# Kernel tuning notes

Hardware: AMD Instinct MI355X
Metric: run time of the kernel (lower is better)

Reference implementation:

```python
import jax, jax.numpy as jnp
import numpy as np

VARIANCES = jnp.array([0.1, 0.1, 0.2, 0.2], jnp.float32)
MAX_TOTAL = 200       # max_total_size
MAX_PER_CLASS = 50    # per-class NMS cap (combined-NMS max_output_size_per_class)
IOU_THR = 0.5
SCORE_THR = 0.5       # score_threshold
EPS = 1e-8


def setup_inputs() -> dict:
    key = jax.random.key(0)
    k1, k2, kc, kh = jax.random.split(key, 4)
    B, N, C = 16, 24564, 81
    pred_deltas = jax.random.normal(k1, (B, N, 4), jnp.float32)
    pred_labels = jax.random.uniform(k2, (B, N, C), jnp.float32)
    # realistic normalized priors: centers uniform in [0,1], sizes ~ [0.02, 0.22]
    ctr = jax.random.uniform(kc, (N, 2), jnp.float32)
    hw = jax.random.uniform(kh, (N, 2), jnp.float32) * 0.2 + 0.02
    y1x1 = jnp.clip(ctr - hw / 2, 0.0, 1.0)
    y2x2 = jnp.clip(ctr + hw / 2, 0.0, 1.0)
    prior_boxes = jnp.concatenate([y1x1, y2x2], axis=-1)  # (N,4) y1x1y2x2
    return {"pred_deltas": pred_deltas, "pred_labels": pred_labels, "prior_boxes": prior_boxes}


def _decode(deltas, priors):
    # deltas: (B,N,4) already scaled by variances; priors: (N,4) y1x1y2x2
    ph = priors[:, 2] - priors[:, 0]
    pw = priors[:, 3] - priors[:, 1]
    pcy = priors[:, 0] + 0.5 * ph
    pcx = priors[:, 1] + 0.5 * pw
    cy = deltas[..., 0] * ph + pcy
    cx = deltas[..., 1] * pw + pcx
    h = jnp.exp(deltas[..., 2]) * ph
    w = jnp.exp(deltas[..., 3]) * pw
    boxes = jnp.stack([cy - h / 2, cx - w / 2, cy + h / 2, cx + w / 2], axis=-1)
    return jnp.clip(boxes, 0.0, 1.0)  # combined NMS clip_boxes=True


def _iou_one_vs_all(box, boxes):
    # box: (4,), boxes: (N,4)
    iy1 = jnp.maximum(box[0], boxes[:, 0])
    ix1 = jnp.maximum(box[1], boxes[:, 1])
    iy2 = jnp.minimum(box[2], boxes[:, 2])
    ix2 = jnp.minimum(box[3], boxes[:, 3])
    inter = jnp.maximum(iy2 - iy1, 0.0) * jnp.maximum(ix2 - ix1, 0.0)
    a0 = (box[2] - box[0]) * (box[3] - box[1])
    a1 = (boxes[:, 2] - boxes[:, 0]) * (boxes[:, 3] - boxes[:, 1])
    return inter / (a0 + a1 - inter + EPS)


def _nms_indices(boxes, scores):
    # greedy NMS on one class: boxes (N,4), scores (N,) -> (K,) idx, (K,) valid
    def body(i, st):
        sc, idx, val = st
        j = jnp.argmax(sc)
        s = sc[j]
        iou = _iou_one_vs_all(boxes[j], boxes)
        sc = jnp.where(iou > IOU_THR, 0.0, sc).at[j].set(0.0)
        return sc, idx.at[i].set(j.astype(jnp.int32)), val.at[i].set(s > SCORE_THR)

    _, idx, val = jax.lax.fori_loop(
        0, MAX_PER_CLASS, body,
        (scores, jnp.zeros(MAX_PER_CLASS, jnp.int32), jnp.zeros(MAX_PER_CLASS, bool)))
    return idx, val


def reference(pred_deltas, pred_labels, prior_boxes):
    B = pred_deltas.shape[0]
    C = pred_labels.shape[-1]
    # 1) delta * variance scaling
    deltas = pred_deltas * VARIANCES
    # 2) background masking: zero all class scores where argmax class == 0
    lab_map = jnp.argmax(pred_labels, axis=-1, keepdims=True)  # (B,N,1)
    scores = jnp.where(lab_map != 0, pred_labels, jnp.zeros_like(pred_labels))  # (B,N,C)
    # 3) box decode (shared across classes, q=1)
    boxes = _decode(deltas, prior_boxes)  # (B,N,4)
    # 4) per-class greedy NMS (combined NMS)
    scores_cn = jnp.swapaxes(scores, 1, 2)  # (B,C,N)
    boxes_sg = jax.lax.stop_gradient(boxes)
    scores_sg = jax.lax.stop_gradient(scores_cn)
    per_class = jax.vmap(lambda bx, sc: jax.vmap(_nms_indices, in_axes=(None, 0))(bx, sc))
    idx, val = per_class(boxes_sg, scores_sg)  # (B,C,K) int32, (B,C,K) bool
    # 5) gather kept detections, merge across classes, keep global top MAX_TOTAL
    sel_scores = jnp.take_along_axis(scores_cn, idx, axis=2) * val  # (B,C,K)
    flat_scores = sel_scores.reshape(B, C * MAX_PER_CLASS)
    flat_idx = idx.reshape(B, C * MAX_PER_CLASS)
    top_scores, top_pos = jax.lax.top_k(flat_scores, MAX_TOTAL)  # (B,200)
    box_idx = jnp.take_along_axis(flat_idx, top_pos, axis=1)  # (B,200)
    sel_boxes = jnp.take_along_axis(boxes, box_idx[..., None], axis=1)  # (B,200,4)
    valid_mask = top_scores > 0.0
    sel_boxes = sel_boxes * valid_mask[..., None].astype(sel_boxes.dtype)
    sel_classes = (top_pos // MAX_PER_CLASS).astype(jnp.float32) * valid_mask
    valid_count = jnp.sum(valid_mask, axis=1).astype(jnp.int32)  # (B,)
    return sel_boxes, top_scores, sel_classes, valid_count
```

## Files before the change

### kernel.cpp

```cpp
#include <hip/hip_runtime.h>
#include <math.h>

#define BB 16
#define NN 24564
#define CC 81
#define KK 50
#define MT 200
#define NROWS (BB * NN)
#define RB 384
#define CAND_CAP 512
#define T1 0.995f
#define T1C0 0.975f
#define TIER_W 0.02f
#define PADI 32
#define CHUNK 128

typedef unsigned long long u64;
typedef unsigned int u32;

__device__ __forceinline__ u64 pack_cand(float s, int n) {
    return ((u64)__float_as_uint(s) << 32) | (u32)(~(u32)n);
}

template <int P, int NT>
__device__ __forceinline__ void bitonic_desc(u64* a, int tid) {
    for (int k = 2; k <= P; k <<= 1) {
        for (int j = k >> 1; j > 0; j >>= 1) {
            for (int i = tid; i < P; i += NT) {
                int l = i ^ j;
                if (l > i) {
                    u64 x = a[i], y = a[l];
                    bool sw = (i & k) ? (x > y) : (x < y);
                    if (sw) { a[i] = y; a[l] = x; }
                }
            }
            __syncthreads();
        }
    }
}

__global__ __launch_bounds__(256) void k_zero(int* __restrict__ cnt_g)
{
    int i = blockIdx.x * 256 + threadIdx.x;
    if (i < BB * CC) cnt_g[i * PADI] = 0;
}

__global__ __launch_bounds__(128) void k_decode_filter(
    const float* __restrict__ deltas, const float* __restrict__ labels,
    const float* __restrict__ priors, float4* __restrict__ boxes,
    unsigned char* __restrict__ bg, int* __restrict__ cnt_g,
    u64* __restrict__ cand_g)
{
    __shared__ float4 lab4[1296];
    __shared__ u64 s_mask[2][CC];
    __shared__ int s_base[2][CC];

    int tid = threadIdx.x;
    int w = tid >> 6, lane = tid & 63;
    int b = blockIdx.x / RB, blk = blockIdx.x - b * RB;
    int row0 = blk * 64;
    int rows = NN - row0; if (rows > 64) rows = 64;
    const float4* src = (const float4*)(labels + ((size_t)b * NN + row0) * CC);
    int nf4 = rows * CC / 4;

    int nfull = nf4 >> 6;
    for (int j = w; j < nfull; j += 2) {
        __builtin_amdgcn_global_load_lds(
            (const __attribute__((address_space(1))) void*)(src + (j << 6) + lane),
            (__attribute__((address_space(3))) void*)(lab4 + (j << 6)),
            16, 0, 0);
    }
    int idx = (nfull << 6) + tid;
    bool hasrem = idx < nf4;
    float4 tv;
    if (hasrem) tv = src[idx];
    asm volatile("s_waitcnt vmcnt(0)" ::: "memory");
    if (hasrem) lab4[idx] = tv;
    __syncthreads();

    int row = lane & 31, h = lane >> 5;
    int rl = w * 32 + row;
    bool inb = rl < rows;
    int n = row0 + rl;
    const float* L = (const float*)lab4 + rl * CC;

    int c0 = h ? 41 : 0, c1 = h ? 81 : 41;
    float L0 = L[0];
    float mq = L[c0];
    u64 win = 0;
    for (int c = c0; c < c1; ++c) {
        float v = L[c];
        mq = fmaxf(mq, v);
        float th = (c == 0) ? T1C0 : T1;
        if (v > th) win |= 1ull << (c - c0);
    }
    float rm = fmaxf(mq, __shfl_xor(mq, 32));
    bool isbg = (L0 >= rm);
    if (inb && h == 0) bg[(size_t)b * NN + n] = isbg ? 1 : 0;
    if (!inb || isbg) win = 0;

    u64 w0 = h ? (win << 41) : win;
    u32 w1 = h ? (u32)(win >> 23) : 0u;

    u64 u0 = w0; u32 u1 = w1;
    #pragma unroll
    for (int off = 1; off < 64; off <<= 1) {
        u0 |= __shfl_xor(u0, off);
        u1 |= __shfl_xor(u1, off);
    }

    s_mask[w][lane] = 0ull;
    if (lane < CC - 64) s_mask[w][64 + lane] = 0ull;

    u64 t0u = u0;
    while (t0u) {
        int c = __ffsll(t0u) - 1; t0u &= t0u - 1;
        u64 mm = __ballot((w0 >> c) & 1);
        if (lane == 0) s_mask[w][c] = mm;
    }
    u32 t1u = u1;
    while (t1u) {
        int j = __ffs(t1u) - 1; t1u &= t1u - 1;
        u64 mm = __ballot((w1 >> j) & 1);
        if (lane == 0) s_mask[w][64 + j] = mm;
    }

    {
        u64 mk = s_mask[w][lane];
        int v2 = 0;
        if (mk) v2 = atomicAdd(&cnt_g[(b * CC + lane) * PADI], (int)__popcll(mk));
        s_base[w][lane] = v2;
        int c3 = 64 + lane;
        if (c3 < CC) {
            u64 mk3 = s_mask[w][c3];
            int v3 = 0;
            if (mk3) v3 = atomicAdd(&cnt_g[(b * CC + c3) * PADI], (int)__popcll(mk3));
            s_base[w][c3] = v3;
        }
    }

    u64 ltmask = (lane == 63) ? 0x7FFFFFFFFFFFFFFFull : ((1ull << lane) - 1ull);
    u64 wrem = win;
    while (wrem) {
        int j = __ffsll(wrem) - 1;
        wrem &= wrem - 1;
        int c = h * 41 + j;
        u64 mm = s_mask[w][c];
        int p = s_base[w][c] + (int)__popcll(mm & ltmask);
        if (p < CAND_CAP)
            cand_g[(size_t)(b * CC + c) * CAND_CAP + p] = pack_cand(L[c], n);
    }

    if (inb && h == 0) {
        size_t r = (size_t)b * NN + n;
        float4 pr = ((const float4*)priors)[n];
        float ph  = __fsub_rn(pr.z, pr.x);
        float pw  = __fsub_rn(pr.w, pr.y);
        float pcy = __fadd_rn(pr.x, __fmul_rn(0.5f, ph));
        float pcx = __fadd_rn(pr.y, __fmul_rn(0.5f, pw));
        float4 dl = ((const float4*)deltas)[r];
        float d0 = __fmul_rn(dl.x, 0.1f);
        float d1 = __fmul_rn(dl.y, 0.1f);
        float d2 = __fmul_rn(dl.z, 0.2f);
        float d3 = __fmul_rn(dl.w, 0.2f);
        float cy = __fadd_rn(__fmul_rn(d0, ph), pcy);
        float cx = __fadd_rn(__fmul_rn(d1, pw), pcx);
        float hh = __fmul_rn(expf(d2), ph);
        float ww = __fmul_rn(expf(d3), pw);
        float h2 = __fmul_rn(hh, 0.5f);
        float w2 = __fmul_rn(ww, 0.5f);
        float y1 = fminf(fmaxf(__fsub_rn(cy, h2), 0.0f), 1.0f);
        float x1 = fminf(fmaxf(__fsub_rn(cx, w2), 0.0f), 1.0f);
        float y2 = fminf(fmaxf(__fadd_rn(cy, h2), 0.0f), 1.0f);
        float x2 = fminf(fmaxf(__fadd_rn(cx, w2), 0.0f), 1.0f);
        boxes[r] = make_float4(y1, x1, y2, x2);
    }
}

__global__ __launch_bounds__(256) void k_nms(
    const float* __restrict__ labels, const unsigned char* __restrict__ bg,
    const float4* __restrict__ boxes, const int* __restrict__ cnt_g,
    const u64* __restrict__ cand_g,
    float* __restrict__ out_s, int* __restrict__ out_i)
{
    __shared__ u64 arr[CAND_CAP];
    __shared__ float4 sbox[CHUNK];
    __shared__ float ks[KK];
    __shared__ int   ki[KK];
    __shared__ int s_kept, s_cnt;

    int bc = blockIdx.x, tid = threadIdx.x;
    int b = bc / CC, c = bc - b * CC;
    float thrc = (c == 0) ? T1C0 : T1;
    const float4* bxb = boxes + (size_t)b * NN;

    int gcnt = cnt_g[bc * PADI];
    bool ovf = gcnt > CAND_CAP;
    int cnt0 = ovf ? 0 : gcnt;
    for (int i = tid; i < CAND_CAP; i += 256)
        arr[i] = (i < cnt0) ? cand_g[(size_t)bc * CAND_CAP + i] : 0ull;
    if (tid == 0) { s_kept = 0; s_cnt = cnt0; }
    __syncthreads();

    float4 kb = make_float4(0.f, 0.f, 0.f, 0.f);
    float  ka = 0.0f;
    float hi = ovf ? 1.0001f : thrc;
    float bw = TIER_W;
    bool first = !ovf;

    while (true) {
        if (!first) {
            if (s_kept >= KK || hi <= 0.5f) break;
            float lo = fmaxf(hi - bw, 0.5f);
            if (tid == 0) s_cnt = 0;
            __syncthreads();
            const float* lab = labels + (size_t)b * NN * CC + c;
            const unsigned char* bgb = bg + (size_t)b * NN;
            for (int n = tid; n < NN; n += 256) {
                float v = lab[(size_t)n * CC];
                if (v > lo && v <= hi && v > 0.5f && !bgb[n]) {
                    int p = atomicAdd(&s_cnt, 1);
                    if (p < CAND_CAP) arr[p] = pack_cand(v, n);
                }
            }
            __syncthreads();
            if (s_cnt > CAND_CAP && bw > 1e-7f) {
                bw *= 0.5f;
                __syncthreads();
                continue;
            }
            int c2 = min(s_cnt, CAND_CAP);
            for (int i = tid; i < CAND_CAP; i += 256)
                if (i >= c2) arr[i] = 0ull;
            hi = lo;
            bw = TIER_W;
            __syncthreads();
        }
        first = false;

        int cs = min(s_cnt, CAND_CAP);
        if (cs <= 128)      bitonic_desc<128, 256>(arr, tid);
        else if (cs <= 256) bitonic_desc<256, 256>(arr, tid);
        else                bitonic_desc<CAND_CAP, 256>(arr, tid);

        for (int ch0 = 0; ch0 < cs; ch0 += CHUNK) {
            if (s_kept >= KK) break;
            int che = min(ch0 + CHUNK, cs);
            for (int i = ch0 + tid; i < che; i += 256) {
                int n = (int)(~(u32)arr[i]);
                if ((u32)n < (u32)NN) sbox[i - ch0] = bxb[n];
            }
            __syncthreads();
            if (tid < 64) {
                int kept = s_kept;
                for (int i = ch0; i < che; ++i) {
                    u64 key = arr[i];
                    float sc = __uint_as_float((u32)(key >> 32));
                    int n = (int)(~(u32)key);
                    float4 cb = sbox[i - ch0];
                    float a1 = __fmul_rn(__fsub_rn(cb.z, cb.x), __fsub_rn(cb.w, cb.y));
                    bool sup = false;
                    if (tid < kept) {
                        float iy1 = fmaxf(kb.x, cb.x);
                        float ix1 = fmaxf(kb.y, cb.y);
                        float iy2 = fminf(kb.z, cb.z);
                        float ix2 = fminf(kb.w, cb.w);
                        float ih = fmaxf(__fsub_rn(iy2, iy1), 0.0f);
                        float iw = fmaxf(__fsub_rn(ix2, ix1), 0.0f);
                        float inter = __fmul_rn(ih, iw);
                        float den = __fadd_rn(__fsub_rn(__fadd_rn(ka, a1), inter), 1e-8f);
                        sup = __fdiv_rn(inter, den) > 0.5f;
                    }
                    if (__ballot(sup) == 0ull) {
                        if (tid == kept) { kb = cb; ka = a1; }
                        if (tid == 0)    { ks[kept] = sc; ki[kept] = n; }
                        ++kept;
                        if (kept == KK) break;
                    }
                }
                if (tid == 0) s_kept = kept;
            }
            __syncthreads();
        }
    }

    int kept = min(s_kept, KK);
    for (int k = tid; k < KK; k += 256) {
        out_s[(size_t)bc * KK + k] = (k < kept) ? ks[k] : 0.0f;
        out_i[(size_t)bc * KK + k] = (k < kept) ? ki[k] : 0;
    }
}

__global__ __launch_bounds__(256) void k_topk1(
    const float* __restrict__ nms_s, u64* __restrict__ topA)
{
    __shared__ u64 arr[512];
    int bchunk = blockIdx.x;
    int b = bchunk >> 3, ch = bchunk & 7;
    int tid = threadIdx.x;
    int base = ch * 512;
    for (int i = tid; i < 512; i += 256) {
        int fp = base + i;
        u64 v = 0ull;
        if (fp < CC * KK) {
            float s = nms_s[(size_t)b * CC * KK + fp];
            v = ((u64)__float_as_uint(s) << 32) | (u32)(~(u32)fp);
        }
        arr[i] = v;
    }
    __syncthreads();
    bitonic_desc<512, 256>(arr, tid);
    if (tid < MT) topA[(size_t)bchunk * MT + tid] = arr[tid];
}

__global__ __launch_bounds__(512) void k_topk2(
    const u64* __restrict__ topA, const int* __restrict__ nms_i,
    const float4* __restrict__ boxes, float* __restrict__ out)
{
    __shared__ u64 arr[2048];
    __shared__ int s_vc;
    int b = blockIdx.x, tid = threadIdx.x;
    for (int i = tid; i < 2048; i += 512)
        arr[i] = (i < 8 * MT) ? topA[(size_t)b * 8 * MT + i] : 0ull;
    if (tid == 0) s_vc = 0;
    __syncthreads();

    bitonic_desc<2048, 512>(arr, tid);

    if (tid < MT) {
        u64 key = arr[tid];
        float sc = __uint_as_float((u32)(key >> 32));
        int fp = (int)(~(u32)key);
        bool valid = sc > 0.0f;
        float4 bb = make_float4(0.f, 0.f, 0.f, 0.f);
        float cls = 0.0f;
        if (valid) {
            int aidx = nms_i[(size_t)b * CC * KK + fp];
            bb = boxes[(size_t)b * NN + aidx];
            cls = (float)(fp / KK);
        }
        ((float4*)out)[(size_t)b * MT + tid] = bb;
        out[(size_t)BB * MT * 4 + (size_t)b * MT + tid] = sc;
        out[(size_t)BB * MT * 5 + (size_t)b * MT + tid] = cls;
        if (valid) atomicAdd(&s_vc, 1);
    }
    __syncthreads();
    if (tid == 0) out[(size_t)BB * MT * 6 + b] = (float)s_vc;
}

extern "C" void kernel_launch(void* const* d_in, const int* in_sizes, int n_in,
                              void* d_out, int out_size, void* d_ws, size_t ws_size,
                              hipStream_t stream)
{
    const float* deltas = (const float*)d_in[0];
    const float* labels = (const float*)d_in[1];
    const float* priors = (const float*)d_in[2];
    float* out = (float*)d_out;

    char* ws = (char*)d_ws;
    size_t off = 0;
    float4* boxes = (float4*)(ws + off);            off += (size_t)NROWS * 16;
    unsigned char* bg = (unsigned char*)(ws + off); off += ((size_t)NROWS + 127) & ~127ull;
    int* cnt_g = (int*)(ws + off);                  off += (size_t)BB * CC * PADI * 4;
    u64* cand_g = (u64*)(ws + off);                 off += (size_t)BB * CC * CAND_CAP * 8;
    float* nms_s = (float*)(ws + off);              off += (size_t)BB * CC * KK * 4;
    int* nms_i = (int*)(ws + off);                  off += (size_t)BB * CC * KK * 4;
    u64* topA = (u64*)(ws + off);                   off += (size_t)BB * 8 * MT * 8;

    k_zero<<<(BB * CC + 255) / 256, 256, 0, stream>>>(cnt_g);
    k_decode_filter<<<BB * RB, 128, 0, stream>>>(deltas, labels, priors,
                                                 boxes, bg, cnt_g, cand_g);
    k_nms<<<BB * CC, 256, 0, stream>>>(labels, bg, boxes, cnt_g, cand_g, nms_s, nms_i);
    k_topk1<<<BB * 8, 256, 0, stream>>>(nms_s, topA);
    k_topk2<<<BB, 512, 0, stream>>>(topA, nms_i, boxes, out);
}
```

Before: 137.9 us.

## Split decode/filter into wave-per-rows filter kernel and separate box decode kernel

```diff
diff --git a/kernel.cpp b/kernel.cpp
--- a/kernel.cpp
+++ b/kernel.cpp
@@ -7,7 +7,6 @@
 #define KK 50
 #define MT 200
 #define NROWS (BB * NN)
-#define RB 384
 #define CAND_CAP 512
 #define T1 0.995f
 #define T1C0 0.975f
@@ -45,136 +44,84 @@
     if (i < BB * CC) cnt_g[i * PADI] = 0;
 }
 
-__global__ __launch_bounds__(128) void k_decode_filter(
-    const float* __restrict__ deltas, const float* __restrict__ labels,
-    const float* __restrict__ priors, float4* __restrict__ boxes,
-    unsigned char* __restrict__ bg, int* __restrict__ cnt_g,
-    u64* __restrict__ cand_g)
-{
-    __shared__ float4 lab4[1296];
-    __shared__ u64 s_mask[2][CC];
-    __shared__ int s_base[2][CC];
-
-    int tid = threadIdx.x;
-    int w = tid >> 6, lane = tid & 63;
-    int b = blockIdx.x / RB, blk = blockIdx.x - b * RB;
-    int row0 = blk * 64;
-    int rows = NN - row0; if (rows > 64) rows = 64;
-    const float4* src = (const float4*)(labels + ((size_t)b * NN + row0) * CC);
-    int nf4 = rows * CC / 4;
-
-    int nfull = nf4 >> 6;
-    for (int j = w; j < nfull; j += 2) {
-        __builtin_amdgcn_global_load_lds(
-            (const __attribute__((address_space(1))) void*)(src + (j << 6) + lane),
-            (__attribute__((address_space(3))) void*)(lab4 + (j << 6)),
-            16, 0, 0);
-    }
-    int idx = (nfull << 6) + tid;
-    bool hasrem = idx < nf4;
-    float4 tv;
-    if (hasrem) tv = src[idx];
-    asm volatile("s_waitcnt vmcnt(0)" ::: "memory");
-    if (hasrem) lab4[idx] = tv;
-    __syncthreads();
-
-    int row = lane & 31, h = lane >> 5;
-    int rl = w * 32 + row;
-    bool inb = rl < rows;
-    int n = row0 + rl;
-    const float* L = (const float*)lab4 + rl * CC;
-
-    int c0 = h ? 41 : 0, c1 = h ? 81 : 41;
-    float L0 = L[0];
-    float mq = L[c0];
-    u64 win = 0;
-    for (int c = c0; c < c1; ++c) {
-        float v = L[c];
-        mq = fmaxf(mq, v);
-        float th = (c == 0) ? T1C0 : T1;
-        if (v > th) win |= 1ull << (c - c0);
-    }
-    float rm = fmaxf(mq, __shfl_xor(mq, 32));
-    bool isbg = (L0 >= rm);
-    if (inb && h == 0) bg[(size_t)b * NN + n] = isbg ? 1 : 0;
-    if (!inb || isbg) win = 0;
-
-    u64 w0 = h ? (win << 41) : win;
-    u32 w1 = h ? (u32)(win >> 23) : 0u;
-
-    u64 u0 = w0; u32 u1 = w1;
-    #pragma unroll
-    for (int off = 1; off < 64; off <<= 1) {
-        u0 |= __shfl_xor(u0, off);
-        u1 |= __shfl_xor(u1, off);
-    }
-
-    s_mask[w][lane] = 0ull;
-    if (lane < CC - 64) s_mask[w][64 + lane] = 0ull;
-
-    u64 t0u = u0;
-    while (t0u) {
-        int c = __ffsll(t0u) - 1; t0u &= t0u - 1;
-        u64 mm = __ballot((w0 >> c) & 1);
-        if (lane == 0) s_mask[w][c] = mm;
-    }
-    u32 t1u = u1;
-    while (t1u) {
-        int j = __ffs(t1u) - 1; t1u &= t1u - 1;
-        u64 mm = __ballot((w1 >> j) & 1);
-        if (lane == 0) s_mask[w][64 + j] = mm;
-    }
-
-    {
-        u64 mk = s_mask[w][lane];
-        int v2 = 0;
-        if (mk) v2 = atomicAdd(&cnt_g[(b * CC + lane) * PADI], (int)__popcll(mk));
-        s_base[w][lane] = v2;
-        int c3 = 64 + lane;
-        if (c3 < CC) {
-            u64 mk3 = s_mask[w][c3];
-            int v3 = 0;
-            if (mk3) v3 = atomicAdd(&cnt_g[(b * CC + c3) * PADI], (int)__popcll(mk3));
-            s_base[w][c3] = v3;
-        }
-    }
-
-    u64 ltmask = (lane == 63) ? 0x7FFFFFFFFFFFFFFFull : ((1ull << lane) - 1ull);
-    u64 wrem = win;
-    while (wrem) {
-        int j = __ffsll(wrem) - 1;
-        wrem &= wrem - 1;
-        int c = h * 41 + j;
-        u64 mm = s_mask[w][c];
-        int p = s_base[w][c] + (int)__popcll(mm & ltmask);
-        if (p < CAND_CAP)
-            cand_g[(size_t)(b * CC + c) * CAND_CAP + p] = pack_cand(L[c], n);
-    }
-
-    if (inb && h == 0) {
-        size_t r = (size_t)b * NN + n;
-        float4 pr = ((const float4*)priors)[n];
-        float ph  = __fsub_rn(pr.z, pr.x);
-        float pw  = __fsub_rn(pr.w, pr.y);
-        float pcy = __fadd_rn(pr.x, __fmul_rn(0.5f, ph));
-        float pcx = __fadd_rn(pr.y, __fmul_rn(0.5f, pw));
-        float4 dl = ((const float4*)deltas)[r];
-        float d0 = __fmul_rn(dl.x, 0.1f);
-        float d1 = __fmul_rn(dl.y, 0.1f);
-        float d2 = __fmul_rn(dl.z, 0.2f);
-        float d3 = __fmul_rn(dl.w, 0.2f);
-        float cy = __fadd_rn(__fmul_rn(d0, ph), pcy);
-        float cx = __fadd_rn(__fmul_rn(d1, pw), pcx);
-        float hh = __fmul_rn(expf(d2), ph);
-        float ww = __fmul_rn(expf(d3), pw);
-        float h2 = __fmul_rn(hh, 0.5f);
-        float w2 = __fmul_rn(ww, 0.5f);
-        float y1 = fminf(fmaxf(__fsub_rn(cy, h2), 0.0f), 1.0f);
-        float x1 = fminf(fmaxf(__fsub_rn(cx, w2), 0.0f), 1.0f);
-        float y2 = fminf(fmaxf(__fadd_rn(cy, h2), 0.0f), 1.0f);
-        float x2 = fminf(fmaxf(__fadd_rn(cx, w2), 0.0f), 1.0f);
-        boxes[r] = make_float4(y1, x1, y2, x2);
-    }
+__global__ __launch_bounds__(256) void k_filter(
+    const float* __restrict__ labels, unsigned char* __restrict__ bg,
+    int* __restrict__ cnt_g, u64* __restrict__ cand_g)
+{
+    int wid = (blockIdx.x * 256 + threadIdx.x) >> 6;
+    int lane = threadIdx.x & 63;
+    int base = wid * 32;
+    if (base >= NROWS) return;
+
+    u32 bgbits = 0;
+    #pragma unroll 4
+    for (int i = 0; i < 32; ++i) {
+        int r = base + i;
+        const float* L = labels + (size_t)r * CC;
+        float v1 = L[lane];
+        float v2 = (lane < CC - 64) ? L[64 + lane] : -1.0f;
+        float m = fmaxf(v1, v2);
+        #pragma unroll
+        for (int off = 1; off < 64; off <<= 1)
+            m = fmaxf(m, __shfl_xor(m, off));
+        float L0 = __shfl(v1, 0);
+        bool isbg = (L0 >= m);
+        bgbits |= (isbg ? 1u : 0u) << i;
+        if (!isbg) {
+            int b = r / NN;
+            int n = r - b * NN;
+            float th1 = (lane == 0) ? T1C0 : T1;
+            if (v1 > th1) {
+                int p = atomicAdd(&cnt_g[(b * CC + lane) * PADI], 1);
+                if (p < CAND_CAP)
+                    cand_g[(size_t)(b * CC + lane) * CAND_CAP + p] = pack_cand(v1, n);
+            }
+            if (lane < CC - 64 && v2 > T1) {
+                int c = 64 + lane;
+                int p = atomicAdd(&cnt_g[(b * CC + c) * PADI], 1);
+                if (p < CAND_CAP)
+                    cand_g[(size_t)(b * CC + c) * CAND_CAP + p] = pack_cand(v2, n);
+            }
+        }
+    }
+    if (lane < 8) {
+        u32 wv = 0;
+        #pragma unroll
+        for (int j = 0; j < 4; ++j)
+            wv |= ((bgbits >> (4 * lane + j)) & 1u) << (8 * j);
+        *(u32*)(bg + base + 4 * lane) = wv;
+    }
+}
+
+__global__ __launch_bounds__(256) void k_boxes(
+    const float* __restrict__ deltas, const float* __restrict__ priors,
+    float4* __restrict__ boxes)
+{
+    int r = blockIdx.x * 256 + threadIdx.x;
+    if (r >= NROWS) return;
+    int b = r / NN;
+    int n = r - b * NN;
+    float4 pr = ((const float4*)priors)[n];
+    float4 dl = ((const float4*)deltas)[r];
+    float ph  = __fsub_rn(pr.z, pr.x);
+    float pw  = __fsub_rn(pr.w, pr.y);
+    float pcy = __fadd_rn(pr.x, __fmul_rn(0.5f, ph));
+    float pcx = __fadd_rn(pr.y, __fmul_rn(0.5f, pw));
+    float d0 = __fmul_rn(dl.x, 0.1f);
+    float d1 = __fmul_rn(dl.y, 0.1f);
+    float d2 = __fmul_rn(dl.z, 0.2f);
+    float d3 = __fmul_rn(dl.w, 0.2f);
+    float cy = __fadd_rn(__fmul_rn(d0, ph), pcy);
+    float cx = __fadd_rn(__fmul_rn(d1, pw), pcx);
+    float hh = __fmul_rn(expf(d2), ph);
+    float ww = __fmul_rn(expf(d3), pw);
+    float h2 = __fmul_rn(hh, 0.5f);
+    float w2 = __fmul_rn(ww, 0.5f);
+    float y1 = fminf(fmaxf(__fsub_rn(cy, h2), 0.0f), 1.0f);
+    float x1 = fminf(fmaxf(__fsub_rn(cx, w2), 0.0f), 1.0f);
+    float y2 = fminf(fmaxf(__fadd_rn(cy, h2), 0.0f), 1.0f);
+    float x2 = fminf(fmaxf(__fadd_rn(cx, w2), 0.0f), 1.0f);
+    boxes[r] = make_float4(y1, x1, y2, x2);
 }
 
 __global__ __launch_bounds__(256) void k_nms(
@@ -368,8 +315,8 @@
     u64* topA = (u64*)(ws + off);                   off += (size_t)BB * 8 * MT * 8;
 
     k_zero<<<(BB * CC + 255) / 256, 256, 0, stream>>>(cnt_g);
-    k_decode_filter<<<BB * RB, 128, 0, stream>>>(deltas, labels, priors,
-                                                 boxes, bg, cnt_g, cand_g);
+    k_filter<<<(NROWS / 32 + 3) / 4, 256, 0, stream>>>(labels, bg, cnt_g, cand_g);
+    k_boxes<<<(NROWS + 255) / 256, 256, 0, stream>>>(deltas, priors, boxes);
     k_nms<<<BB * CC, 256, 0, stream>>>(labels, bg, boxes, cnt_g, cand_g, nms_s, nms_i);
     k_topk1<<<BB * 8, 256, 0, stream>>>(nms_s, topA);
     k_topk2<<<BB, 512, 0, stream>>>(topA, nms_i, boxes, out);
```

Result: slower. 156.7 us (+13.6%).
